# Kernel optimization log

Measured on AMD Instinct MI355X. Metric: run time of the kernel, lower is better.

The kernel has to match this reference:

```python
import jax, jax.numpy as jnp
import numpy as np
from jax import lax

B, CIN, HF, WF = 8, 512, 60, 60      # encoder feature
NCLS = 19                            # seg out channels
PATCH = 10                           # patch_size
DEPTH = 8                            # 2**att_depth
UPS = 8                              # seg upsampling
HI = HF * UPS                        # 480 upsampled image size
NP_IMG = (HI // PATCH) ** 2          # 2304 image patches
NP_FEA = (HI // DEPTH // PATCH) ** 2 # 36 feature patches
POOL_SIZES = (1, 2, 3, 6)


def resize_ac(x, H, W):
    # bilinear, align_corners=True (matches F.interpolate/UpsamplingBilinear2d)
    b, c, h, w = x.shape
    ys = jnp.arange(H, dtype=x.dtype) * ((h - 1) / max(H - 1, 1))
    xs = jnp.arange(W, dtype=x.dtype) * ((w - 1) / max(W - 1, 1))
    y0 = jnp.floor(ys).astype(jnp.int32); y1 = jnp.minimum(y0 + 1, h - 1)
    x0 = jnp.floor(xs).astype(jnp.int32); x1 = jnp.minimum(x0 + 1, w - 1)
    wy = (ys - y0.astype(x.dtype))[:, None]
    wx = (xs - x0.astype(x.dtype))[None, :]
    g = lambda yi, xi: x[:, :, yi[:, None], xi[None, :]]
    top = (1 - wx) * g(y0, x0) + wx * g(y0, x1)
    bot = (1 - wx) * g(y1, x0) + wx * g(y1, x1)
    return (1 - wy) * top + wy * bot


def bn_eval(x, gamma, beta, mean, var, eps=1e-5):
    s = lambda v: v[None, :, None, None]
    return (x - s(mean)) * (s(gamma) / jnp.sqrt(s(var) + eps)) + s(beta)


def setup_inputs() -> dict:
    key = jax.random.key(0)
    ks = jax.random.split(key, 16)
    f32 = jnp.float32
    return {
        "feat": jax.random.normal(ks[0], (B, CIN, HF, WF), f32),
        "attentions": jax.random.normal(ks[1], (B, NCLS, NP_IMG, NP_FEA), f32),
        "w_psp": jax.random.normal(ks[2], (4, CIN // 4, CIN), f32) * 0.03,
        "b_psp0": jax.random.normal(ks[3], (CIN // 4,), f32) * 0.02,
        "bn_psp_gamma": jax.random.uniform(ks[4], (3, CIN // 4), f32, 0.5, 1.5),
        "bn_psp_beta": jax.random.normal(ks[5], (3, CIN // 4), f32) * 0.02,
        "bn_psp_mean": jax.random.normal(ks[6], (3, CIN // 4), f32) * 0.02,
        "bn_psp_var": jax.random.uniform(ks[7], (3, CIN // 4), f32, 0.5, 1.5),
        "w_conv": jax.random.normal(ks[8], (512, 2 * CIN), f32) * 0.03,
        "bn_conv_gamma": jax.random.uniform(ks[9], (512,), f32, 0.5, 1.5),
        "bn_conv_beta": jax.random.normal(ks[10], (512,), f32) * 0.02,
        "bn_conv_mean": jax.random.normal(ks[11], (512,), f32) * 0.02,
        "bn_conv_var": jax.random.uniform(ks[12], (512,), f32, 0.5, 1.5),
        "w_segconv": jax.random.normal(ks[13], (NCLS, 512, 3, 3), f32) * 0.03,
        "b_segconv": jax.random.normal(ks[14], (NCLS,), f32) * 0.02,
    }


def _forward(feat, attentions, w_psp, b_psp0, bn_psp_gamma, bn_psp_beta,
             bn_psp_mean, bn_psp_var, w_conv, bn_conv_gamma, bn_conv_beta,
             bn_conv_mean, bn_conv_var, w_segconv, b_segconv):
    # ---- PSP pyramid ----
    branches = []
    for i, p in enumerate(POOL_SIZES):
        k = HF // p
        pooled = feat.reshape(B, CIN, p, k, p, k).mean(axis=(3, 5))  # adaptive avg pool
        y = jnp.einsum('oc,bchw->bohw', w_psp[i], pooled)
        if i == 0:  # pool_size==1 -> no BN, conv has bias
            y = y + b_psp0[None, :, None, None]
        else:
            y = bn_eval(y, bn_psp_gamma[i-1], bn_psp_beta[i-1],
                        bn_psp_mean[i-1], bn_psp_var[i-1])
        y = jax.nn.relu(y)
        branches.append(resize_ac(y, HF, WF))
    x = jnp.concatenate(branches + [feat], axis=1)  # [B, 2*CIN, HF, WF]

    # ---- 1x1 Conv2dReLU + BN (eval), dropout is identity in eval ----
    x = jnp.einsum('oc,bchw->bohw', w_conv, x)
    x = jax.nn.relu(bn_eval(x, bn_conv_gamma, bn_conv_beta, bn_conv_mean, bn_conv_var))

    # ---- SegmentationHead ----
    x = lax.conv_general_dilated(x, w_segconv, (1, 1), 'SAME',
                                 dimension_numbers=('NCHW', 'OIHW', 'NCHW'))
    x = x + b_segconv[None, :, None, None]
    x = resize_ac(x, HI, HI)  # [B, NCLS, 480, 480]

    # one-hot of per-pixel argmax (scatter of ones)
    am = jnp.argmax(x, axis=1)
    x_softmax = (am[:, None] == jnp.arange(NCLS)[None, :, None, None]).astype(x.dtype)

    # grouped ones-conv stride 8 / 64 == 8x8 average pooling
    hf = HI // DEPTH  # 60
    argx_feamap = x_softmax.reshape(B, NCLS, hf, DEPTH, hf, DEPTH).mean(axis=(3, 5))

    # unfold(k=10, s=10): [B, C, 36, 100] (blocks row-major, patch row-major)
    nb = hf // PATCH  # 6
    unf = argx_feamap.reshape(B, NCLS, nb, PATCH, nb, PATCH)
    unf = unf.transpose(0, 1, 2, 4, 3, 5).reshape(B, NCLS, nb * nb, PATCH * PATCH)

    counts = jnp.count_nonzero(attentions, axis=-1, keepdims=True).astype(x.dtype) + 1e-5
    att = jnp.einsum('bcpk,bckq->bcpq', attentions / counts, unf)  # [B,C,2304,100]

    # fold back to [B, C, 480, 480]
    nbi = HI // PATCH  # 48
    corr = att.reshape(B, NCLS, nbi, nbi, PATCH, PATCH)
    corr = corr.transpose(0, 1, 2, 4, 3, 5).reshape(B, NCLS, HI, HI)

    x = corr * x + x  # activation=None -> identity
    return x, attentions


def reference(feat, attentions, w_psp, b_psp0, bn_psp_gamma, bn_psp_beta,
              bn_psp_mean, bn_psp_var, w_conv, bn_conv_gamma, bn_conv_beta,
              bn_conv_mean, bn_conv_var, w_segconv, b_segconv):
    return _forward(feat, attentions, w_psp, b_psp0, bn_psp_gamma, bn_psp_beta,
                    bn_psp_mean, bn_psp_var, w_conv, bn_conv_gamma, bn_conv_beta,
                    bn_conv_mean, bn_conv_var, w_segconv, b_segconv)
```

## Files before the change

### kernel.cpp

```cpp
#include <hip/hip_runtime.h>
#include <stdint.h>

#define NB 8
#define NCLS 19

typedef short s8v __attribute__((ext_vector_type(8)));
typedef float f4v __attribute__((ext_vector_type(4)));

__device__ __forceinline__ unsigned short f2b(float f){
  union { float f; uint32_t u; } v; v.f = f;
  uint32_t u = v.u;
  uint32_t r = (u + 0x7fffu + ((u >> 16) & 1u)) >> 16;
  return (unsigned short)r;
}

#define GLOAD16(g, l) __builtin_amdgcn_global_load_lds( \
    (const __attribute__((address_space(1))) unsigned int*)(g), \
    (__attribute__((address_space(3))) unsigned int*)(l), 16, 0, 0)

#define OFF_X512 0
#define OFF_POOL 31490048
#define OFF_Z    32309248
#define OFF_BNS  33128448
#define OFF_BNB  33130496
#define OFF_SEG  33132544
#define OFF_ARGX 35321344
#define OFF_WSEG 37510144
#define OFF_WF   37805056

__global__ __launch_bounds__(256) void k_setup(
    const float* __restrict__ feat, unsigned short* __restrict__ featT,
    unsigned short* __restrict__ x512p,
    const float* __restrict__ wseg, unsigned short* __restrict__ wsegT,
    const float* __restrict__ wconv, unsigned short* __restrict__ wfT,
    const float* __restrict__ g, const float* __restrict__ be,
    const float* __restrict__ m, const float* __restrict__ v,
    float* __restrict__ sc, float* __restrict__ sh,
    unsigned short* __restrict__ argxT)
{
  __shared__ unsigned short lt[64*528];
  int bid = blockIdx.x;
  if (bid < 456){
    int b = bid / 57, px0 = (bid - b*57)*64;
    for (int i = threadIdx.x; i < 64*512; i += 256){
      int c = i >> 6, px = i & 63;
      float val = feat[((size_t)b*512 + c)*3600 + min(px0+px, 3599)];
      lt[px*528 + c] = f2b(val);
    }
    __syncthreads();
    for (int i = threadIdx.x; i < 4096; i += 256){
      int px = i >> 6, c8 = i & 63;
      s8v vv = *(const s8v*)(lt + px*528 + c8*8);
      *(s8v*)(featT + ((size_t)b*3712 + px0 + px)*512 + c8*8) = vv;
    }
    return;
  }
  bid -= 456;
  if (bid < 488){
    int idx = bid*256 + threadIdx.x;
    if (idx < 124928){
      int pix = idx >> 6;
      int ch  = (idx & 63) << 3;
      int b = pix / 244;
      int r = pix - b*244;
      int h, w;
      if (r < 62){ h = 0; w = r; }
      else if (r < 124){ h = 61; w = r - 62; }
      else if (r < 184){ h = r - 124 + 1; w = 0; }
      else { h = r - 184 + 1; w = 61; }
      s8v z = (s8v){0,0,0,0,0,0,0,0};
      *(s8v*)(x512p + (((size_t)b*62 + h)*62 + w)*512 + ch) = z;
    }
    return;
  }
  bid -= 488;
  if (bid < 576){
    int idx = bid*256 + threadIdx.x;
    if (idx < 9*32*512){
      int tap = idx / (32*512);
      int rem = idx - tap*(32*512);
      int o = rem >> 9, c = rem & 511;
      float val = (o < NCLS) ? wseg[((size_t)o*512 + c)*9 + tap] : 0.0f;
      wsegT[idx] = f2b(val);
    }
    return;
  }
  bid -= 576;
  if (bid < 1024){
    int idx = bid*256 + threadIdx.x;
    if (idx < 512*512){
      int o = idx >> 9, c = idx & 511;
      wfT[idx] = f2b(wconv[(size_t)o*1024 + 512 + c]);
    }
    return;
  }
  bid -= 1024;
  if (bid < 2){
    int i = bid*256 + threadIdx.x;
    if (i < 512){
      float s = g[i] * rsqrtf(v[i] + 1e-5f);
      sc[i] = s; sh[i] = be[i] - m[i]*s;
    }
    return;
  }
  bid -= 2;
  {
    int gi = bid*256 + threadIdx.x;
    if (gi < 136192){
      s8v z = (s8v){0,0,0,0,0,0,0,0};
      ((s8v*)argxT)[gi] = z;
    }
  }
}

__global__ void k0_copy(const float4* __restrict__ in, float4* __restrict__ out, int n4){
  for (int i = blockIdx.x*blockDim.x + threadIdx.x; i < n4; i += gridDim.x*blockDim.x)
    out[i] = in[i];
}

__global__ __launch_bounds__(64) void k1_pool(const float* __restrict__ feat, float* __restrict__ pooled){
  int bc = blockIdx.x;
  __shared__ float rs[64][12];
  int r = threadIdx.x;
  if (r < 60){
    const float* row = feat + (size_t)bc*3600 + r*60;
    float s6[6];
    #pragma unroll
    for (int j = 0; j < 6; j++){
      float s = 0.f;
      #pragma unroll
      for (int i = 0; i < 10; i++) s += row[j*10+i];
      s6[j] = s;
    }
    float s3_0 = s6[0]+s6[1], s3_1 = s6[2]+s6[3], s3_2 = s6[4]+s6[5];
    float s2_0 = s3_0 + s6[2], s2_1 = s6[3] + s3_2;
    rs[r][0]  = s2_0 + s2_1;
    rs[r][1]  = s2_0; rs[r][2]  = s2_1;
    rs[r][3]  = s3_0; rs[r][4]  = s3_1; rs[r][5] = s3_2;
    #pragma unroll
    for (int j = 0; j < 6; j++) rs[r][6+j] = s6[j];
  }
  __syncthreads();
  int t = threadIdx.x;
  if (t < 50){
    int P, by, bx, jcol;
    if (t == 0){ P=1; by=0; bx=0; jcol=0; }
    else if (t < 5){ P=2; int l=t-1; by=l>>1; bx=l&1; jcol=1+bx; }
    else if (t < 14){ P=3; int l=t-5; by=l/3; bx=l-(l/3)*3; jcol=3+bx; }
    else { P=6; int l=t-14; by=l/6; bx=l-(l/6)*6; jcol=6+bx; }
    int k = 60/P;
    float s = 0.f;
    for (int rr = 0; rr < k; rr++) s += rs[by*k+rr][jcol];
    pooled[(size_t)bc*50 + t] = s * (1.0f/((float)k*(float)k));
  }
}

__global__ __launch_bounds__(256) void k2_branch(
    const float* __restrict__ pooled, const float* __restrict__ w_psp,
    const float* __restrict__ b_psp0,
    const float* __restrict__ png, const float* __restrict__ pnb,
    const float* __restrict__ pnm, const float* __restrict__ pnv,
    const float* __restrict__ wconv, float* __restrict__ zbuf)
{
  int bin = blockIdx.x % 50;
  int b   = blockIdx.x / 50;
  int br  = (bin < 1) ? 0 : (bin < 5) ? 1 : (bin < 14) ? 2 : 3;
  __shared__ float pl[512];
  __shared__ float ysh[128];
  int t = threadIdx.x;
  pl[t]       = pooled[((size_t)b*512 + t)*50 + bin];
  pl[t + 256] = pooled[((size_t)b*512 + t + 256)*50 + bin];
  __syncthreads();
  if (t < 128){
    const float* wr = w_psp + ((size_t)br*128 + t)*512;
    float s = 0.f;
    #pragma unroll 8
    for (int c = 0; c < 512; c++) s += pl[c]*wr[c];
    if (br == 0) s += b_psp0[t];
    else {
      int ib = (br-1)*128 + t;
      s = (s - pnm[ib]) * png[ib] * rsqrtf(pnv[ib] + 1e-5f) + pnb[ib];
    }
    ysh[t] = fmaxf(s, 0.f);
  }
  __syncthreads();
  for (int o = t; o < 512; o += 256){
    const float* wc = wconv + (size_t)o*1024 + br*128;
    float s = 0.f;
    #pragma unroll
    for (int c = 0; c < 128; c++) s += ysh[c]*wc[c];
    zbuf[((size_t)b*50 + bin)*512 + o] = s;
  }
}

__global__ __launch_bounds__(256) void k3_gemm(
    const unsigned short* __restrict__ featT, const unsigned short* __restrict__ wfT,
    const float* __restrict__ zbuf, const float* __restrict__ bns,
    const float* __restrict__ bnb, unsigned short* __restrict__ x512p)
{
  __shared__ unsigned short lmem[2*128*64];
  unsigned short* lA = lmem;
  unsigned short* lB = lmem + 128*64;

  const int t = threadIdx.x;
  const int lane = t & 63;
  const int wave = t >> 6;
  const int wm = wave >> 1;
  const int wn = wave & 1;
  const int pix0 = blockIdx.x * 128;
  const int o0   = blockIdx.y * 128;
  const int b    = blockIdx.z;

  f4v acc[4][4];
  #pragma unroll
  for (int i = 0; i < 4; i++)
    #pragma unroll
    for (int j = 0; j < 4; j++)
      acc[i][j] = (f4v){0.f,0.f,0.f,0.f};

  const int sub  = lane >> 3;
  const int slot = lane & 7;

  for (int kk = 0; kk < 8; kk++){
    #pragma unroll
    for (int j = 0; j < 4; j++){
      int px = j*32 + wave*8 + sub;
      int pix = min(pix0 + px, 3599);
      const unsigned short* src = featT + ((size_t)b*3712 + pix)*512 + kk*64 + ((slot ^ (px & 7)) << 3);
      GLOAD16(src, lA + j*2048 + wave*512);
    }
    #pragma unroll
    for (int j = 0; j < 4; j++){
      int o = j*32 + wave*8 + sub;
      const unsigned short* src = wfT + (size_t)(o0 + o)*512 + kk*64 + ((slot ^ (o & 7)) << 3);
      GLOAD16(src, lB + j*2048 + wave*512);
    }
    __syncthreads();
    #pragma unroll
    for (int ks = 0; ks < 2; ks++){
      const int chunk = ks*4 + (lane >> 4);
      s8v af[4], bg[4];
      #pragma unroll
      for (int mf = 0; mf < 4; mf++){
        int p = wm*64 + mf*16 + (lane & 15);
        af[mf] = *(s8v*)((char*)lA + p*128 + ((chunk ^ (p & 7)))*16);
      }
      #pragma unroll
      for (int nf = 0; nf < 4; nf++){
        int o = wn*64 + nf*16 + (lane & 15);
        bg[nf] = *(s8v*)((char*)lB + o*128 + ((chunk ^ (o & 7)))*16);
      }
      #pragma unroll
      for (int mf = 0; mf < 4; mf++)
        #pragma unroll
        for (int nf = 0; nf < 4; nf++)
          acc[mf][nf] = __builtin_amdgcn_mfma_f32_16x16x32_bf16(af[mf], bg[nf], acc[mf][nf], 0, 0, 0);
    }
    __syncthreads();
  }

  float* zl  = (float*)lmem;
  float* lsc = zl + 50*128;
  float* lsh = lsc + 128;
  for (int i = t; i < 50*128; i += 256){
    int bin = i >> 7, ol = i & 127;
    zl[i] = zbuf[((size_t)b*50 + bin)*512 + o0 + ol];
  }
  if (t < 128){ lsc[t] = bns[o0 + t]; lsh[t] = bnb[o0 + t]; }
  __syncthreads();

  #pragma unroll
  for (int mf = 0; mf < 4; mf++){
    #pragma unroll
    for (int r = 0; r < 4; r++){
      int p = pix0 + wm*64 + mf*16 + (lane >> 4)*4 + r;
      if (p >= 3600) continue;
      int h = p / 60, w = p - (p/60)*60;
      float wgt[3][4]; int bix[3][4];
      const int pbase[3] = {1,5,14};
      const int psz[3]   = {2,3,6};
      #pragma unroll
      for (int ib = 0; ib < 3; ib++){
        int P = psz[ib];
        float fy = (float)h * (float)(P-1) / 59.0f;
        float fx = (float)w * (float)(P-1) / 59.0f;
        int y0 = (int)fy; int y1 = min(y0+1, P-1); float wy = fy - (float)y0;
        int x0 = (int)fx; int x1 = min(x0+1, P-1); float wx = fx - (float)x0;
        bix[ib][0] = pbase[ib] + y0*P + x0; wgt[ib][0] = (1.f-wy)*(1.f-wx);
        bix[ib][1] = pbase[ib] + y0*P + x1; wgt[ib][1] = (1.f-wy)*wx;
        bix[ib][2] = pbase[ib] + y1*P + x0; wgt[ib][2] = wy*(1.f-wx);
        bix[ib][3] = pbase[ib] + y1*P + x1; wgt[ib][3] = wy*wx;
      }
      size_t obase = (((size_t)b*62 + (h+1))*62 + (w+1))*512 + o0;
      #pragma unroll
      for (int nf = 0; nf < 4; nf++){
        int ol = wn*64 + nf*16 + (lane & 15);
        float zs = zl[ol];
        #pragma unroll
        for (int ib = 0; ib < 3; ib++)
          #pragma unroll
          for (int tp = 0; tp < 4; tp++)
            zs += wgt[ib][tp] * zl[bix[ib][tp]*128 + ol];
        float v = acc[mf][nf][r] + zs;
        v = fmaxf(v * lsc[ol] + lsh[ol], 0.f);
        x512p[obase + ol] = f2b(v);
      }
    }
  }
}

__global__ __launch_bounds__(256) void k4_conv(
    const unsigned short* __restrict__ x512p, const unsigned short* __restrict__ wsegT,
    const float* __restrict__ bseg, float* __restrict__ seg60)
{
  __shared__ unsigned short lW[32*512];
  const int h = blockIdx.x;
  const int b = blockIdx.y;
  const int t = threadIdx.x;
  const int lane = t & 63;
  const int wave = t >> 6;
  const int wpix = wave*16 + (lane & 15);
  const int wld = min(wpix, 59);

  f4v acc[2];
  acc[0] = (f4v){0.f,0.f,0.f,0.f};
  acc[1] = (f4v){0.f,0.f,0.f,0.f};

  for (int tap = 0; tap < 9; tap++){
    __syncthreads();
    for (int i = t; i < 2048; i += 256){
      int orow = i >> 6;
      int cn = i & 63;
      s8v v = *(const s8v*)(wsegT + ((size_t)tap*32 + orow)*512 + cn*8);
      *(s8v*)((char*)lW + orow*1024 + ((cn ^ (orow & 7)))*16) = v;
    }
    __syncthreads();
    int dy = tap/3 - 1, dx = tap - (tap/3)*3 - 1;
    const unsigned short* arow = x512p + (((size_t)b*62 + (h+dy+1))*62 + (wld+dx+1))*512 + (lane>>4)*8;
    #pragma unroll 4
    for (int cs = 0; cs < 16; cs++){
      int cb = cs*32;
      s8v a = *(const s8v*)(arow + cb);
      #pragma unroll
      for (int nf = 0; nf < 2; nf++){
        int o = nf*16 + (lane & 15);
        int chunk = (cb >> 3) + (lane >> 4);
        s8v bv = *(s8v*)((char*)lW + o*1024 + ((chunk ^ (o & 7)))*16);
        acc[nf] = __builtin_amdgcn_mfma_f32_16x16x32_bf16(a, bv, acc[nf], 0, 0, 0);
      }
    }
  }
  #pragma unroll
  for (int nf = 0; nf < 2; nf++){
    int o = nf*16 + (lane & 15);
    if (o < NCLS){
      float bias = bseg[o];
      #pragma unroll
      for (int r = 0; r < 4; r++){
        int wst = wave*16 + (lane >> 4)*4 + r;
        if (wst < 60)
          seg60[(((size_t)b*60 + h)*60 + wst)*NCLS + o] = acc[nf][r] + bias;
      }
    }
  }
}

__global__ __launch_bounds__(256) void k5_argmax(const float* __restrict__ seg60, unsigned short* __restrict__ argxT){
  int gw = blockIdx.x*4 + (threadIdx.x >> 6);
  int b = gw / 3600;
  int cell = gw - b*3600;
  int fy = cell / 60, fx = cell - (cell/60)*60;
  int lane = threadIdx.x & 63;
  int py = fy*8 + (lane >> 3), px = fx*8 + (lane & 7);
  float yy = (float)py * (59.0f/479.0f); int y0 = (int)yy; int y1 = min(y0+1, 59); float wy = yy - (float)y0;
  float xx = (float)px * (59.0f/479.0f); int x0 = (int)xx; int x1 = min(x0+1, 59); float wx = xx - (float)x0;
  const float* base = seg60 + (size_t)b*3600*NCLS;
  const float* s00 = base + (y0*60 + x0)*NCLS;
  const float* s01 = base + (y0*60 + x1)*NCLS;
  const float* s10 = base + (y1*60 + x0)*NCLS;
  const float* s11 = base + (y1*60 + x1)*NCLS;
  float w00 = (1.f-wy)*(1.f-wx), w01 = (1.f-wy)*wx, w10 = wy*(1.f-wx), w11 = wy*wx;
  float best = -3.0e38f; int bc = 0;
  #pragma unroll
  for (int c = 0; c < NCLS; c++){
    float v = w00*s00[c] + w01*s01[c] + w10*s10[c] + w11*s11[c];
    if (v > best){ best = v; bc = c; }
  }
  int cnt = 0;
  #pragma unroll
  for (int c = 0; c < NCLS; c++){
    unsigned long long m = __ballot(bc == c);
    if (lane == c) cnt = __popcll(m);
  }
  int ky = fy/10, qy = fy - (fy/10)*10, kx = fx/10, qx = fx - (fx/10)*10;
  int q = qy*10 + qx, k = ky*6 + kx;
  if (lane < NCLS){
    unsigned short hv = f2b((float)cnt * (1.0f/64.0f));
    argxT[(size_t)(b*NCLS + lane)*7168 + q*64 + (((k>>3) ^ (q&7))<<3) + (k&7)] = hv;
  }
}

__global__ __launch_bounds__(256) void k7_final(
    const float* __restrict__ att, const unsigned short* __restrict__ argxT,
    const float* __restrict__ seg60, float* __restrict__ out)
{
  int pr = blockIdx.x, c = blockIdx.y, b = blockIdx.z;
  __shared__ char pool[30400];
  unsigned short* Abf = (unsigned short*)pool;
  unsigned short* Ubf = (unsigned short*)(pool + 6144);
  float* corrl = (float*)pool;
  float* hrow  = (float*)(pool + 21504);
  float* inv   = (float*)(pool + 29184);
  float* srow  = (float*)(pool + 29376);
  const int t = threadIdx.x;
  const int lane = t & 63;
  const int wave = t >> 6;

  int ybase; { float yy0 = (float)(pr*10)*(59.0f/479.0f); ybase = (int)yy0; }

  const float* ab = att + (((size_t)b*NCLS + c)*2304 + (size_t)pr*48)*36;
  for (int i = t; i < 768; i += 256){
    int pc = i >> 4, j = i & 15;
    ushort4 w4 = make_ushort4(0,0,0,0);
    if (j < 9){
      f4v v = *(const f4v*)(ab + pc*36 + j*4);
      w4.x = f2b(v[0]); w4.y = f2b(v[1]); w4.z = f2b(v[2]); w4.w = f2b(v[3]);
    }
    int ch = j >> 1;
    *(ushort4*)((char*)Abf + pc*128 + (((ch ^ (pc & 7)))<<4) + (j & 1)*8) = w4;
  }
  {
    const unsigned short* up = argxT + (size_t)(b*NCLS + c)*7168;
    #pragma unroll
    for (int r = 0; r < 4; r++){
      int chunk0 = r*256 + wave*64;
      if (chunk0 < 896)
        GLOAD16(up + (size_t)(chunk0 + lane)*8, Ubf + (size_t)chunk0*8);
    }
  }
  if (t < 240){
    int j = t/60, x = t - (t/60)*60;
    int row = min(ybase + j, 59);
    srow[j*64 + x] = seg60[(((size_t)b*60 + row)*60 + x)*NCLS + c];
  }
  if (t < 48){
    int nz = 0;
    #pragma unroll
    for (int j2 = 0; j2 < 9; j2++){
      f4v v = *(const f4v*)(ab + t*36 + j2*4);
      nz += (v[0]!=0.f)+(v[1]!=0.f)+(v[2]!=0.f)+(v[3]!=0.f);
    }
    inv[t] = 1.0f/((float)nz + 1e-5f);
  }
  __syncthreads();

  f4v acc[6];
  #pragma unroll
  for (int s = 0; s < 6; s++) acc[s] = (f4v){0.f,0.f,0.f,0.f};
  #pragma unroll
  for (int s = 0; s < 6; s++){
    int pi = wave + s*4;
    if (pi < 21){
      int M = pi/7, N = pi - (pi/7)*7;
      #pragma unroll
      for (int ks = 0; ks < 2; ks++){
        int chunk = ks*4 + (lane >> 4);
        int ar = M*16 + (lane & 15);
        s8v af = *(s8v*)((char*)Abf + ar*128 + ((chunk ^ (ar & 7))<<4));
        int qr = N*16 + (lane & 15);
        s8v bg = *(s8v*)((char*)Ubf + qr*128 + ((chunk ^ (qr & 7))<<4));
        acc[s] = __builtin_amdgcn_mfma_f32_16x16x32_bf16(af, bg, acc[s], 0, 0, 0);
      }
    }
  }
  __syncthreads();

  #pragma unroll
  for (int s = 0; s < 6; s++){
    int pi = wave + s*4;
    if (pi < 21){
      int M = pi/7, N = pi - (pi/7)*7;
      int q = N*16 + (lane & 15);
      #pragma unroll
      for (int r = 0; r < 4; r++){
        int pc = M*16 + (lane >> 4)*4 + r;
        corrl[pc*112 + q] = acc[s][r] * inv[pc];
      }
    }
  }
  for (int i = t; i < 1920; i += 256){
    int j = i/480, px = i - (i/480)*480;
    float xx = (float)px * (59.0f/479.0f);
    int x0 = (int)xx; int x1 = min(x0+1, 59); float wx = xx - (float)x0;
    hrow[j*480 + px] = (1.f-wx)*srow[j*64 + x0] + wx*srow[j*64 + x1];
  }
  __syncthreads();

  float* outb = out + ((size_t)b*NCLS + c)*230400 + (size_t)pr*4800;
  for (int qy = 0; qy < 10; qy++){
    int py = pr*10 + qy;
    float yy = (float)py * (59.0f/479.0f);
    int y0 = (int)yy; int y1 = min(y0+1, 59); float wy = yy - (float)y0;
    const float* h0 = hrow + (y0 - ybase)*480;
    const float* h1 = hrow + (y1 - ybase)*480;
    float omw = 1.f - wy;
    for (int px = t; px < 480; px += 256){
      float xv = omw*h0[px] + wy*h1[px];
      int pc = (px*6554) >> 16;
      int qx = px - pc*10;
      float corr = corrl[pc*112 + qy*10 + qx];
      outb[qy*480 + px] = xv * (1.f + corr);
    }
  }
}

extern "C" void kernel_launch(void* const* d_in, const int* in_sizes, int n_in,
                              void* d_out, int out_size, void* d_ws, size_t ws_size,
                              hipStream_t stream)
{
  (void)in_sizes; (void)n_in; (void)out_size; (void)ws_size;
  const float* feat   = (const float*)d_in[0];
  const float* attn   = (const float*)d_in[1];
  const float* w_psp  = (const float*)d_in[2];
  const float* b_psp0 = (const float*)d_in[3];
  const float* png    = (const float*)d_in[4];
  const float* pnb    = (const float*)d_in[5];
  const float* pnm    = (const float*)d_in[6];
  const float* pnv    = (const float*)d_in[7];
  const float* wconv  = (const float*)d_in[8];
  const float* cg     = (const float*)d_in[9];
  const float* cbt    = (const float*)d_in[10];
  const float* cm     = (const float*)d_in[11];
  const float* cv     = (const float*)d_in[12];
  const float* wseg   = (const float*)d_in[13];
  const float* bseg   = (const float*)d_in[14];

  float* out1 = (float*)d_out;
  float* out2 = out1 + (size_t)35020800;

  char* ws = (char*)d_ws;
  unsigned short* x512p = (unsigned short*)(ws + OFF_X512);
  float* pooled = (float*)(ws + OFF_POOL);
  float* zbuf   = (float*)(ws + OFF_Z);
  float* bns    = (float*)(ws + OFF_BNS);
  float* bnb    = (float*)(ws + OFF_BNB);
  float* seg60  = (float*)(ws + OFF_SEG);
  unsigned short* argxT = (unsigned short*)(ws + OFF_ARGX);
  unsigned short* wsegT = (unsigned short*)(ws + OFF_WSEG);
  unsigned short* wfT   = (unsigned short*)(ws + OFF_WF);
  unsigned short* featT = (unsigned short*)d_out;

  k_setup<<<3078, 256, 0, stream>>>(feat, featT, x512p, wseg, wsegT, wconv, wfT,
                                    cg, cbt, cm, cv, bns, bnb, argxT);
  k1_pool<<<4096, 64, 0, stream>>>(feat, pooled);
  k2_branch<<<400, 256, 0, stream>>>(pooled, w_psp, b_psp0, png, pnb, pnm, pnv, wconv, zbuf);
  k3_gemm<<<dim3(29,4,8), 256, 0, stream>>>(featT, wfT, zbuf, bns, bnb, x512p);
  k0_copy<<<2048, 256, 0, stream>>>((const float4*)attn, (float4*)out2, 12607488/4);
  k4_conv<<<dim3(60,8), 256, 0, stream>>>(x512p, wsegT, bseg, seg60);
  k5_argmax<<<7200, 256, 0, stream>>>(seg60, argxT);
  k7_final<<<dim3(48,19,8), 256, 0, stream>>>(attn, argxT, seg60, out1);
}
```

Before: 273.9 us.

## Fuse attention passthrough copy into final kernel and keep bilinear rows in registers

```diff
diff --git a/kernel.cpp b/kernel.cpp
--- a/kernel.cpp
+++ b/kernel.cpp
@@ -113,11 +113,6 @@
   }
 }
 
-__global__ void k0_copy(const float4* __restrict__ in, float4* __restrict__ out, int n4){
-  for (int i = blockIdx.x*blockDim.x + threadIdx.x; i < n4; i += gridDim.x*blockDim.x)
-    out[i] = in[i];
-}
-
 __global__ __launch_bounds__(64) void k1_pool(const float* __restrict__ feat, float* __restrict__ pooled){
   int bc = blockIdx.x;
   __shared__ float rs[64][12];
@@ -402,28 +397,30 @@
 
 __global__ __launch_bounds__(256) void k7_final(
     const float* __restrict__ att, const unsigned short* __restrict__ argxT,
-    const float* __restrict__ seg60, float* __restrict__ out)
+    const float* __restrict__ seg60, float* __restrict__ out, float* __restrict__ out2)
 {
   int pr = blockIdx.x, c = blockIdx.y, b = blockIdx.z;
-  __shared__ char pool[30400];
+  __shared__ char pool[22720];
   unsigned short* Abf = (unsigned short*)pool;
   unsigned short* Ubf = (unsigned short*)(pool + 6144);
   float* corrl = (float*)pool;
-  float* hrow  = (float*)(pool + 21504);
-  float* inv   = (float*)(pool + 29184);
-  float* srow  = (float*)(pool + 29376);
+  float* inv   = (float*)(pool + 21504);
+  float* srow  = (float*)(pool + 21696);
   const int t = threadIdx.x;
   const int lane = t & 63;
   const int wave = t >> 6;
 
   int ybase; { float yy0 = (float)(pr*10)*(59.0f/479.0f); ybase = (int)yy0; }
 
-  const float* ab = att + (((size_t)b*NCLS + c)*2304 + (size_t)pr*48)*36;
+  const size_t aoff = (((size_t)b*NCLS + c)*2304 + (size_t)pr*48)*36;
+  const float* ab = att + aoff;
+  float* o2 = out2 + aoff;
   for (int i = t; i < 768; i += 256){
     int pc = i >> 4, j = i & 15;
     ushort4 w4 = make_ushort4(0,0,0,0);
     if (j < 9){
       f4v v = *(const f4v*)(ab + pc*36 + j*4);
+      *(f4v*)(o2 + pc*36 + j*4) = v;
       w4.x = f2b(v[0]); w4.y = f2b(v[1]); w4.z = f2b(v[2]); w4.w = f2b(v[3]);
     }
     int ch = j >> 1;
@@ -473,6 +470,19 @@
       }
     }
   }
+  float hA[4], hB[4];
+  {
+    float xxa = (float)t * (59.0f/479.0f);
+    int xa0 = (int)xxa; int xa1 = min(xa0+1, 59); float wxa = xxa - (float)xa0;
+    int px2 = t + 256;
+    float xxb = (float)px2 * (59.0f/479.0f);
+    int xb0 = (int)xxb; int xb1 = min(xb0+1, 59); float wxb = xxb - (float)xb0;
+    #pragma unroll
+    for (int j = 0; j < 4; j++){
+      hA[j] = (1.f-wxa)*srow[j*64 + xa0] + wxa*srow[j*64 + xa1];
+      hB[j] = (px2 < 480) ? ((1.f-wxb)*srow[j*64 + xb0] + wxb*srow[j*64 + xb1]) : 0.f;
+    }
+  }
   __syncthreads();
 
   #pragma unroll
@@ -488,28 +498,28 @@
       }
     }
   }
-  for (int i = t; i < 1920; i += 256){
-    int j = i/480, px = i - (i/480)*480;
-    float xx = (float)px * (59.0f/479.0f);
-    int x0 = (int)xx; int x1 = min(x0+1, 59); float wx = xx - (float)x0;
-    hrow[j*480 + px] = (1.f-wx)*srow[j*64 + x0] + wx*srow[j*64 + x1];
-  }
   __syncthreads();
 
   float* outb = out + ((size_t)b*NCLS + c)*230400 + (size_t)pr*4800;
+  int pcA = (t*6554) >> 16, qxA = t - pcA*10;
+  int px2 = t + 256;
+  int pcB = (px2*6554) >> 16, qxB = px2 - pcB*10;
+  #pragma unroll
   for (int qy = 0; qy < 10; qy++){
     int py = pr*10 + qy;
     float yy = (float)py * (59.0f/479.0f);
     int y0 = (int)yy; int y1 = min(y0+1, 59); float wy = yy - (float)y0;
-    const float* h0 = hrow + (y0 - ybase)*480;
-    const float* h1 = hrow + (y1 - ybase)*480;
+    int j0 = y0 - ybase, j1 = y1 - ybase;
+    float h0a = (j0==0)?hA[0]:(j0==1)?hA[1]:(j0==2)?hA[2]:hA[3];
+    float h1a = (j1==0)?hA[0]:(j1==1)?hA[1]:(j1==2)?hA[2]:hA[3];
     float omw = 1.f - wy;
-    for (int px = t; px < 480; px += 256){
-      float xv = omw*h0[px] + wy*h1[px];
-      int pc = (px*6554) >> 16;
-      int qx = px - pc*10;
-      float corr = corrl[pc*112 + qy*10 + qx];
-      outb[qy*480 + px] = xv * (1.f + corr);
+    float xv = omw*h0a + wy*h1a;
+    outb[qy*480 + t] = xv * (1.f + corrl[pcA*112 + qy*10 + qxA]);
+    if (px2 < 480){
+      float h0b = (j0==0)?hB[0]:(j0==1)?hB[1]:(j0==2)?hB[2]:hB[3];
+      float h1b = (j1==0)?hB[0]:(j1==1)?hB[1]:(j1==2)?hB[2]:hB[3];
+      float xv2 = omw*h0b + wy*h1b;
+      outb[qy*480 + px2] = xv2 * (1.f + corrl[pcB*112 + qy*10 + qxB]);
     }
   }
 }
@@ -555,8 +565,7 @@
   k1_pool<<<4096, 64, 0, stream>>>(feat, pooled);
   k2_branch<<<400, 256, 0, stream>>>(pooled, w_psp, b_psp0, png, pnb, pnm, pnv, wconv, zbuf);
   k3_gemm<<<dim3(29,4,8), 256, 0, stream>>>(featT, wfT, zbuf, bns, bnb, x512p);
-  k0_copy<<<2048, 256, 0, stream>>>((const float4*)attn, (float4*)out2, 12607488/4);
   k4_conv<<<dim3(60,8), 256, 0, stream>>>(x512p, wsegT, bseg, seg60);
   k5_argmax<<<7200, 256, 0, stream>>>(seg60, argxT);
-  k7_final<<<dim3(48,19,8), 256, 0, stream>>>(attn, argxT, seg60, out1);
-}
+  k7_final<<<dim3(48,19,8), 256, 0, stream>>>(attn, argxT, seg60, out1, out2);
+}
```

Result: faster. 263.8 us (-3.7%).
